# Performance work log

Hardware: AMD Instinct MI355X
Metric: run time of the kernel (lower is better)

Reference implementation:

```python
import jax, jax.numpy as jnp
import numpy as np
from jax import lax

B, S, V, D, L = 16, 512, 32000, 512, 64


def setup_inputs() -> dict:
    key = jax.random.key(0)
    ks = jax.random.split(key, 6)
    return {
        "token_ids": jax.random.randint(ks[0], (B, S), 0, V),
        "vocab_emb": jax.random.normal(ks[1], (V, D), jnp.float32) * 0.02,
        "pos_W": jax.random.normal(ks[2], (D, L), jnp.float32) * (1.0 / np.sqrt(D)),
        "pos_b": jnp.zeros((L,), jnp.float32),
        "W1": jax.random.normal(ks[3], (2 * D, D), jnp.float32) * (1.0 / np.sqrt(2 * D)),
        "b1": jnp.zeros((D,), jnp.float32),
        "w2": jax.random.normal(ks[4], (D,), jnp.float32) * (1.0 / np.sqrt(D)),
        "b2": jnp.zeros((), jnp.float32),
    }


def reference(token_ids, vocab_emb, pos_W, pos_b, W1, b1, w2, b2):
    feats = vocab_emb[token_ids]                      # (B, S, D) embedding lookup
    logits = feats @ pos_W + pos_b                    # (B, S, L) POS-tag logits
    cls = jnp.argmax(logits, axis=-1)                 # (B, S)

    # same_cls_as_neighbor: sequence-chain neighbors OR same predicted class, no self loops
    idx = jnp.arange(S)
    chain = jnp.abs(idx[:, None] - idx[None, :]) == 1
    not_self = idx[:, None] != idx[None, :]
    same = cls[:, :, None] == cls[:, None, :]
    adj = (chain[None] | same) & not_self[None]       # (B, S, S) bool

    # rnn_linear (2D->D) followed directly by rnn_linear2 (D->1) with no nonlinearity:
    # score(i,j) = w2.(W1a f_i + W1b f_j + b1) + b2 = f_i.u + f_j.v + c  (exact rewrite)
    W1a, W1b = W1[:D], W1[D:]
    u = W1a @ w2
    v = W1b @ w2
    c = b1 @ w2 + b2

    def parse_one(f, a):
        # greedy easy-first merge loop: S-1 merges until one node remains
        def step(carry, _):
            f, a, tot = carry
            si = f @ u                                 # (S,)
            sj = f @ v                                 # (S,)
            sc = jnp.where(a, si[:, None] + sj[None, :] + c, -jnp.inf)  # (S, S)
            k = jnp.argmax(sc)                         # flat argmax over neighbor pairs
            i, j = k // S, k % S
            best = sc.reshape(-1)[k]
            parent = f[i] @ W1a + f[j] @ W1b + b1      # parent feature of merged pair
            f = f.at[i].set(parent)                    # slot i <- parent
            row = a[i] | a[j]                          # parent inherits both neighborhoods
            a = a.at[i, :].set(row).at[:, i].set(row)
            a = a.at[j, :].set(False).at[:, j].set(False)  # slot j removed
            a = a.at[i, i].set(False)
            return (f, a, tot + best), jnp.stack([i, j])

        (_, _, tot), tree = lax.scan(step, (f, a, jnp.float32(0.0)), None, length=S - 1)
        return tot, tree

    total_score, parse_tree = jax.vmap(parse_one)(feats, adj)
    return total_score, parse_tree                    # (B,), (B, S-1, 2)
```

## Files before the change

### kernel.cpp

```cpp
#include <hip/hip_runtime.h>

#define cB 16
#define cS 512
#define cD 512
#define cL 64
#define cG 8
#define cT 1024

constexpr size_t FCOPY   = (size_t)cB * cS * cD * 4;
constexpr size_t OFF_F0  = 0;
constexpr size_t OFF_F1  = FCOPY;
constexpr size_t OFF_U   = 2 * FCOPY;
constexpr size_t OFF_V   = OFF_U  + 2048;
constexpr size_t OFF_UA  = OFF_V  + 2048;
constexpr size_t OFF_UB  = OFF_UA + 2048;
constexpr size_t OFF_VA  = OFF_UB + 2048;
constexpr size_t OFF_VB  = OFF_VA + 2048;
constexpr size_t OFF_SC  = OFF_VB + 2048;
constexpr size_t OFF_SI  = OFF_SC + 64;
constexpr size_t OFF_SJ  = OFF_SI + (size_t)cB*cS*4;
constexpr size_t OFF_CLS = OFF_SJ + (size_t)cB*cS*4;
constexpr size_t OFF_ADJ = OFF_CLS+ (size_t)cB*cS*4;
constexpr size_t OFF_RM  = OFF_ADJ+ (size_t)cB*cS*64;
constexpr size_t OFF_RA  = OFF_RM + (size_t)cB*cS*4;
constexpr size_t OFF_BAR = ((OFF_RA + (size_t)cB*cS*4 + 127) & ~(size_t)127);

template <int CTRL, int RMASK>
__device__ __forceinline__ void dpp_max_step(float& v, int& k) {
    const float ov = __int_as_float(__builtin_amdgcn_update_dpp(
        (int)0xff800000u, __float_as_int(v), CTRL, RMASK, 0xf, false));
    const int ok = __builtin_amdgcn_update_dpp(
        0x7fffffff, k, CTRL, RMASK, 0xf, false);
    if (ov > v || (ov == v && ok < k)) { v = ov; k = ok; }
}

__device__ __forceinline__ void wave_max64(float& v, int& k) {
    dpp_max_step<0x111, 0xf>(v, k);
    dpp_max_step<0x112, 0xf>(v, k);
    dpp_max_step<0x114, 0xf>(v, k);
    dpp_max_step<0x118, 0xf>(v, k);
    dpp_max_step<0x142, 0xa>(v, k);
    dpp_max_step<0x143, 0xc>(v, k);
}

template <int N>
__device__ __forceinline__ float dpp_shl_add(float x) {
    const float o = __int_as_float(__builtin_amdgcn_update_dpp(
        0, __float_as_int(x), 0x100 + N , 0xf, 0xf, false));
    return x + o;
}

__global__ void k1_uvc(const float* __restrict__ W1, const float* __restrict__ b1,
                       const float* __restrict__ w2, const float* __restrict__ b2,
                       char* __restrict__ ws) {
    const int t = threadIdx.x;
    const int r = blockIdx.x;
    if (r == 1025) {
        unsigned* bar = (unsigned*)(ws + OFF_BAR);
        for (int i = t; i < 4096; i += 256) bar[i] = 0u;
        return;
    }
    __shared__ float rs[256];
    float acc;
    if (r < 1024) {
        const float* row = W1 + (size_t)r * cD;
        acc = row[t] * w2[t] + row[t + 256] * w2[t + 256];
    } else {
        acc = b1[t] * w2[t] + b1[t + 256] * w2[t + 256];
    }
    rs[t] = acc; __syncthreads();
    for (int o = 128; o; o >>= 1) { if (t < o) rs[t] += rs[t + o]; __syncthreads(); }
    if (t == 0) {
        if (r < 512)        ((float*)(ws + OFF_U))[r] = rs[0];
        else if (r < 1024)  ((float*)(ws + OFF_V))[r - 512] = rs[0];
        else                ((float*)(ws + OFF_SC))[0] = rs[0] + b2[0];
    }
}

__global__ void k1b_proj(const float* __restrict__ W1, const float* __restrict__ b1,
                         char* __restrict__ ws) {
    __shared__ float ru[256], rv[256];
    const int t = threadIdx.x;
    const int k = blockIdx.x;
    const float* U = (const float*)(ws + OFF_U);
    const float* V = (const float*)(ws + OFF_V);
    const float* row = (k < 1024) ? (W1 + (size_t)k * cD) : b1;
    ru[t] = row[t] * U[t] + row[t + 256] * U[t + 256];
    rv[t] = row[t] * V[t] + row[t + 256] * V[t + 256];
    __syncthreads();
    for (int o = 128; o; o >>= 1) {
        if (t < o) { ru[t] += ru[t + o]; rv[t] += rv[t + o]; }
        __syncthreads();
    }
    if (t == 0) {
        if (k < 512)       { ((float*)(ws + OFF_UA))[k] = ru[0]; ((float*)(ws + OFF_VA))[k] = rv[0]; }
        else if (k < 1024) { ((float*)(ws + OFF_UB))[k - 512] = ru[0]; ((float*)(ws + OFF_VB))[k - 512] = rv[0]; }
        else               { ((float*)(ws + OFF_SC))[1] = ru[0]; ((float*)(ws + OFF_SC))[2] = rv[0]; }
    }
}

__global__ void k2_feat(const int* __restrict__ tok, const float* __restrict__ emb,
                        char* __restrict__ ws) {
    __shared__ float ru[256], rv[256];
    const int t = threadIdx.x;
    const int bs = blockIdx.x;
    const float* U = (const float*)(ws + OFF_U);
    const float* V = (const float*)(ws + OFF_V);
    float* F = (float*)(ws + OFF_F0);
    const int tk = tok[bs];
    const float* src = emb + (size_t)tk * cD;
    float* dst = F + (size_t)bs * cD;
    const float e0 = src[t], e1 = src[t + 256];
    dst[t] = e0; dst[t + 256] = e1;
    ru[t] = e0 * U[t] + e1 * U[t + 256];
    rv[t] = e0 * V[t] + e1 * V[t + 256];
    __syncthreads();
    for (int o = 128; o; o >>= 1) {
        if (t < o) { ru[t] += ru[t + o]; rv[t] += rv[t + o]; }
        __syncthreads();
    }
    if (t == 0) {
        ((float*)(ws + OFF_SI))[bs] = ru[0];
        ((float*)(ws + OFF_SJ))[bs] = rv[0];
    }
}

__global__ void k3_cls(const float* __restrict__ posW, const float* __restrict__ posb,
                       char* __restrict__ ws) {
    const int t = threadIdx.x;
    const int bs = blockIdx.x;
    const float* frow = (const float*)(ws + OFF_F0) + (size_t)bs * cD;
    float acc = posb[t];
    for (int k = 0; k < cD; k++) acc += frow[k] * posW[(size_t)k * cL + t];
    int idx = t;
    for (int off = 32; off; off >>= 1) {
        float ov = __shfl_down(acc, off, 64);
        int   oi = __shfl_down(idx, off, 64);
        if (ov > acc || (ov == acc && oi < idx)) { acc = ov; idx = oi; }
    }
    if (t == 0) ((int*)(ws + OFF_CLS))[bs] = idx;
}

__global__ void k4_adj(char* __restrict__ ws) {
    __shared__ float rsv[256]; __shared__ int rsk[256];
    const int t = threadIdx.x;
    const int bs = blockIdx.x;
    const int b = bs >> 9, r = bs & 511;
    const int* cls = (const int*)(ws + OFF_CLS) + (size_t)b * cS;
    const float* SJ = (const float*)(ws + OFF_SJ) + (size_t)b * cS;
    const float sir = ((const float*)(ws + OFF_SI))[bs];
    const float c0 = ((const float*)(ws + OFF_SC))[0];
    unsigned long long* adjrow = (unsigned long long*)(ws + OFF_ADJ) + (size_t)bs * 8;
    const int cr = cls[r];
    float bv = -INFINITY; int bc = 0;
    for (int p = 0; p < 2; p++) {
        const int c = p * 256 + t;
        int dd = c - r; if (dd < 0) dd = -dd;
        const bool allowed = (c != r) && (dd == 1 || cls[c] == cr);
        unsigned long long m = __ballot(allowed);
        if ((t & 63) == 0) adjrow[p * 4 + (t >> 6)] = m;
        if (allowed) {
            float val = sir + SJ[c] + c0;
            if (val > bv || (val == bv && c < bc)) { bv = val; bc = c; }
        }
    }
    rsv[t] = bv; rsk[t] = bc; __syncthreads();
    for (int o = 128; o; o >>= 1) {
        if (t < o) {
            float s2 = rsv[t + o]; int k2 = rsk[t + o];
            if (s2 > rsv[t] || (s2 == rsv[t] && k2 < rsk[t])) { rsv[t] = s2; rsk[t] = k2; }
        }
        __syncthreads();
    }
    if (t == 0) { ((float*)(ws + OFF_RM))[bs] = rsv[0]; ((int*)(ws + OFF_RA))[bs] = rsk[0]; }
}

__global__ void __launch_bounds__(cT, 4)
parse_main(const float* __restrict__ W1, const float* __restrict__ b1,
           char* __restrict__ ws, float* __restrict__ out) {
    const int t  = threadIdx.x;
    const int b  = blockIdx.x & 15;
    const int g  = blockIdx.x >> 4;
    const int d0 = g * 64;
    const int wf = t >> 6;
    const int ln = t & 63;
    const int wv = wf >> 1;
    const int h  = wf & 1;

    unsigned long long* F64[2] = {
        (unsigned long long*)(ws + OFF_F0) + (size_t)b * cS * cD / 2,
        (unsigned long long*)(ws + OFF_F1) + (size_t)b * cS * cD / 2 };
    unsigned* prog = (unsigned*)(ws + OFF_BAR) + (size_t)b * 256;
    const float* SCp = (const float*)(ws + OFF_SC);
    const float c0 = SCp[0], cu_c = SCp[1], cv_c = SCp[2];

    __shared__ unsigned long long AdjL[8 * 512];
    __shared__ float SIl[512], SJl[512], rmax[512];
    __shared__ int   rarg[512];
    __shared__ int   tau[512];
    __shared__ unsigned char par[512];
    __shared__ float rsh[1024];
    __shared__ float wsv[8];  __shared__ int wsk[8];
    __shared__ float ws_si[8], ws_sj[8];
    __shared__ int   s_info;
    __shared__ int   rescanList[516]; __shared__ int nresc;

    const int kbase = wv * 128;
    float wreg[64];
#pragma unroll
    for (int m = 0; m < 32; m++) {
        wreg[2 * m]     = W1[(size_t)(kbase + 4 * m + 2 * h)     * cD + d0 + ln];
        wreg[2 * m + 1] = W1[(size_t)(kbase + 4 * m + 2 * h + 1) * cD + d0 + ln];
    }

    const int xk = (wv & 3) * 128 + 2 * ln;
    float cu0 = 0.f, cu1 = 0.f, cv0 = 0.f, cv1 = 0.f;
    if (h == 0) {
        const float* cu_base = (const float*)(ws + ((wv < 4) ? OFF_UA : OFF_UB));
        const float* cvb     = (const float*)(ws + ((wv < 4) ? OFF_VA : OFF_VB));
        cu0 = cu_base[xk]; cu1 = cu_base[xk + 1];
        cv0 = cvb[xk];     cv1 = cvb[xk + 1];
    }

    if (t < cS) {
        SIl[t]  = ((const float*)(ws + OFF_SI))[b * cS + t];
        SJl[t]  = ((const float*)(ws + OFF_SJ))[b * cS + t];
        rmax[t] = ((const float*)(ws + OFF_RM))[b * cS + t];
        rarg[t] = ((const int*)(ws + OFF_RA))[b * cS + t];
        tau[t]  = -1;
        par[t]  = 0;
        const unsigned long long* AG =
            (const unsigned long long*)(ws + OFF_ADJ) + (size_t)b * cS * 8;
#pragma unroll
        for (int wq = 0; wq < 8; wq++) AdjL[wq * 512 + t] = AG[(size_t)t * 8 + wq];
    }
    float b1v = 0.f;
    if (t < 64) b1v = b1[d0 + t];
    bool myAlive = true;
    float tot = 0.f;
    if (t == 0) nresc = 0;

    if (t < cS) {
        float av = rmax[t]; int ak = (t << 9) | (rarg[t] & 511);
        wave_max64(av, ak);
        if (ln == 63) { wsv[wf] = av; wsk[wf] = ak; }
    }
    __syncthreads();

    for (int it = 0; it < cS - 1; ++it) {
        if (wf == 0) {
            float fv = (ln < 8) ? wsv[ln] : -INFINITY;
            int   fk = (ln < 8) ? wsk[ln] : 0x7fffffff;
            dpp_max_step<0x111, 0xf>(fv, fk);
            dpp_max_step<0x112, 0xf>(fv, fk);
            dpp_max_step<0x114, 0xf>(fv, fk);
            const int bk = __builtin_amdgcn_readlane(fk, 7);
            const int pbi = bk >> 9, pbj = bk & 511;
            const int ti = tau[pbi], tj = tau[pbj];
            const int pi = (int)par[pbi], pj = (int)par[pbj];
            const int need = (ti > tj ? ti : tj) + 1;
            if (need > 0) {
                const unsigned un = (unsigned)need;
                for (;;) {
                    unsigned v = 0xffffffffu;
                    if (ln < 8) v = __hip_atomic_load(prog + ln * 32, __ATOMIC_RELAXED,
                                                      __HIP_MEMORY_SCOPE_AGENT);
                    if (__ballot(v >= un) == ~0ull) break;
                    __builtin_amdgcn_s_sleep(1);
                }
            }
            if (ln == 0) {
                s_info = pbi | (pbj << 9) | (pi << 18) | (pj << 19);
                if (g == 0) {
                    const float bfv = __int_as_float(
                        __builtin_amdgcn_readlane(__float_as_int(fv), 7));
                    tot += bfv;
                    out[16 + b * 1022 + it * 2 + 0] = (float)pbi;
                    out[16 + b * 1022 + it * 2 + 1] = (float)pbj;
                }
            }
        }
        __syncthreads();
        const int info = s_info;
        const int bi = info & 511, bj = (info >> 9) & 511;

        const int myrow  = (wv < 4) ? bi : bj;
        const int mypar  = (wv < 4) ? ((info >> 18) & 1) : ((info >> 19) & 1);
        unsigned long long xv = __hip_atomic_load(
            F64[mypar] + (size_t)myrow * 256 + (wv & 3) * 64 + ln,
            __ATOMIC_RELAXED, __HIP_MEMORY_SCOPE_AGENT);
        float2 f2; __builtin_memcpy(&f2, &xv, 8);
        if (h == 0) {
            float csi = f2.x * cu0 + f2.y * cu1;
            float csj = f2.x * cv0 + f2.y * cv1;
            csi += __shfl_down(csi, 32, 64);  csj += __shfl_down(csj, 32, 64);
            csi += __shfl_down(csi, 16, 64);  csj += __shfl_down(csj, 16, 64);
            csi = dpp_shl_add<8>(csi);  csj = dpp_shl_add<8>(csj);
            csi = dpp_shl_add<4>(csi);  csj = dpp_shl_add<4>(csj);
            csi = dpp_shl_add<2>(csi);  csj = dpp_shl_add<2>(csj);
            csi = dpp_shl_add<1>(csi);  csj = dpp_shl_add<1>(csj);
            if (ln == 0) { ws_si[wv] = csi; ws_sj[wv] = csj; }
        }
        {
            const int ix = __float_as_int(f2.x), iy = __float_as_int(f2.y);
            float aP = 0.f, aQ = 0.f;
            if (h == 0) {
#pragma unroll
                for (int m = 0; m < 32; m++) {
                    const float q0 = __int_as_float(__builtin_amdgcn_readlane(ix, 2 * m));
                    const float q1 = __int_as_float(__builtin_amdgcn_readlane(iy, 2 * m));
                    aP += wreg[2 * m] * q0;
                    aQ += wreg[2 * m + 1] * q1;
                }
            } else {
#pragma unroll
                for (int m = 0; m < 32; m++) {
                    const float q0 = __int_as_float(__builtin_amdgcn_readlane(ix, 2 * m + 1));
                    const float q1 = __int_as_float(__builtin_amdgcn_readlane(iy, 2 * m + 1));
                    aP += wreg[2 * m] * q0;
                    aQ += wreg[2 * m + 1] * q1;
                }
            }
            rsh[t] = aP + aQ;
        }
        __syncthreads();

        if (wf == 0) {
            float p = b1v;
#pragma unroll
            for (int q = 0; q < 8; q++)
                p += rsh[(2 * q) * 64 + ln] + rsh[(2 * q + 1) * 64 + ln];
            __hip_atomic_store((float*)F64[mypar ^ 1] + (size_t)bi * 512 + d0 + ln, p,
                               __ATOMIC_RELAXED, __HIP_MEMORY_SCOPE_AGENT);
        }

        float su = (ln < 8) ? ws_si[ln] : 0.f;
        float sv = (ln < 8) ? ws_sj[ln] : 0.f;
        su = dpp_shl_add<4>(su);  sv = dpp_shl_add<4>(sv);
        su = dpp_shl_add<2>(su);  sv = dpp_shl_add<2>(sv);
        su = dpp_shl_add<1>(su);  sv = dpp_shl_add<1>(sv);
        const float sn = __int_as_float(
            __builtin_amdgcn_readfirstlane(__float_as_int(su))) + cu_c;
        const float jn = __int_as_float(
            __builtin_amdgcn_readfirstlane(__float_as_int(sv))) + cv_c;

        if (t < cS) {
            const float sjn_ = jn;
            const int wbi = bi >> 6, wbj = bj >> 6;
            const unsigned long long mbi = 1ull << (bi & 63), mbj = 1ull << (bj & 63);
            const int r = t;
            if (r == bj) {
                if (myAlive) { myAlive = false; rmax[t] = -INFINITY; }
            } else if (r == bi) {
#pragma unroll
                for (int wq = 0; wq < 8; wq++) {
                    unsigned long long nw = AdjL[wq * 512 + bi] | AdjL[wq * 512 + bj];
                    if (wq == wbi) nw &= ~mbi;
                    if (wq == wbj) nw &= ~mbj;
                    AdjL[wq * 512 + bi] = nw;
                }
                int slot = atomicAdd(&nresc, 1); rescanList[slot] = bi;
                SIl[bi] = sn; SJl[bi] = jn; par[bi] ^= 1; tau[bi] = it;
            } else if (myAlive) {
                unsigned long long wi = AdjL[wbi * 512 + r];
                unsigned long long wj = (wbj == wbi) ? wi : AdjL[wbj * 512 + r];
                const bool nb = ((wi & mbi) | (wj & mbj)) != 0ull;
                if (wbi == wbj) {
                    AdjL[wbi * 512 + r] = (wi & ~(mbi | mbj)) | (nb ? mbi : 0ull);
                } else {
                    AdjL[wbi * 512 + r] = (wi & ~mbi) | (nb ? mbi : 0ull);
                    AdjL[wbj * 512 + r] = wj & ~mbj;
                }
                const int ra = rarg[t];
                if (ra == bi || ra == bj) {
                    int slot = atomicAdd(&nresc, 1); rescanList[slot] = r;
                } else if (nb) {
                    const float val = SIl[r] + sjn_ + c0;
                    if (val > rmax[t] || (val == rmax[t] && bi < ra)) { rmax[t] = val; rarg[t] = bi; }
                }
            }
        }
        if (wf == 0) {
            asm volatile("s_waitcnt vmcnt(0)" ::: "memory");
            if (ln == 0)
                __hip_atomic_store(prog + g * 32, (unsigned)(it + 1), __ATOMIC_RELAXED,
                                   __HIP_MEMORY_SCOPE_AGENT);
        }
        __syncthreads();

        const int nr = nresc;
        for (int q = wf; q < nr; q += 16) {
            const int r = rescanList[q];
            const float sir = SIl[r];
            float bv2 = -INFINITY; int bc2 = 0x7fffffff;
#pragma unroll
            for (int k = 0; k < 8; k++) {
                const unsigned long long word = AdjL[k * 512 + r];
                if ((word >> ln) & 1ull) {
                    const int c = k * 64 + ln;
                    const float val = sir + SJl[c] + c0;
                    if (val > bv2 || (val == bv2 && c < bc2)) { bv2 = val; bc2 = c; }
                }
            }
            wave_max64(bv2, bc2);
            if (ln == 63) { rmax[r] = bv2; rarg[r] = bc2; }
        }
        __syncthreads();

        if (t < cS) {
            float av = rmax[t]; int ak = (t << 9) | (rarg[t] & 511);
            wave_max64(av, ak);
            if (ln == 63) { wsv[wf] = av; wsk[wf] = ak; }
        }
        if (t == 0) nresc = 0;
        __syncthreads();
    }
    if (g == 0 && t == 0) out[b] = tot;
}

extern "C" void kernel_launch(void* const* d_in, const int* in_sizes, int n_in,
                              void* d_out, int out_size, void* d_ws, size_t ws_size,
                              hipStream_t stream) {
    const int*   token_ids = (const int*)d_in[0];
    const float* vocab_emb = (const float*)d_in[1];
    const float* pos_W     = (const float*)d_in[2];
    const float* pos_b     = (const float*)d_in[3];
    const float* W1        = (const float*)d_in[4];
    const float* b1        = (const float*)d_in[5];
    const float* w2        = (const float*)d_in[6];
    const float* b2        = (const float*)d_in[7];
    float* out = (float*)d_out;
    char*  ws  = (char*)d_ws;

    k1_uvc<<<1026, 256, 0, stream>>>(W1, b1, w2, b2, ws);
    k1b_proj<<<1025, 256, 0, stream>>>(W1, b1, ws);
    k2_feat<<<cB * cS, 256, 0, stream>>>(token_ids, vocab_emb, ws);
    k3_cls<<<cB * cS, 64, 0, stream>>>(pos_W, pos_b, ws);
    k4_adj<<<cB * cS, 256, 0, stream>>>(ws);

    void* args[] = { (void*)&W1, (void*)&b1, (void*)&ws, (void*)&out };
    hipLaunchCooperativeKernel((void*)parse_main, dim3(cB * cG), dim3(cT),
                               args, 0, stream);
}
```

Before: 3.035 ms.

## Restructure merge loop to cut a barrier and move parent reduction to idle wave

Removes the per-iteration stage where every wave reduces its row maxima into shared partials. Wave 0 now scans all 512 row maxima itself at the start of the next iteration, which eliminates one __syncthreads per merge step. The parent-feature reduction, global store and progress flag move to wave 15, which does no adjacency update, so that work runs alongside the adjacency update instead of before it. It also caches the last observed progress level to skip redundant spin polls, drops the s_sleep in the spin loop, and uses explicit fmaf with paired weights. The trade-off is a serial 8-element scan per lane on wave 0 and more aggressive polling traffic on the progress counters.

```diff
diff --git a/kernel.cpp b/kernel.cpp
--- a/kernel.cpp
+++ b/kernel.cpp
@@ -200,17 +200,16 @@
     __shared__ int   tau[512];
     __shared__ unsigned char par[512];
     __shared__ float rsh[1024];
-    __shared__ float wsv[8];  __shared__ int wsk[8];
     __shared__ float ws_si[8], ws_sj[8];
     __shared__ int   s_info;
     __shared__ int   rescanList[516]; __shared__ int nresc;
 
     const int kbase = wv * 128;
-    float wreg[64];
+    float2 wreg2[32];
 #pragma unroll
     for (int m = 0; m < 32; m++) {
-        wreg[2 * m]     = W1[(size_t)(kbase + 4 * m + 2 * h)     * cD + d0 + ln];
-        wreg[2 * m + 1] = W1[(size_t)(kbase + 4 * m + 2 * h + 1) * cD + d0 + ln];
+        wreg2[m].x = W1[(size_t)(kbase + 4 * m + 2 * h)     * cD + d0 + ln];
+        wreg2[m].y = W1[(size_t)(kbase + 4 * m + 2 * h + 1) * cD + d0 + ln];
     }
 
     const int xk = (wv & 3) * 128 + 2 * ln;
@@ -235,45 +234,45 @@
         for (int wq = 0; wq < 8; wq++) AdjL[wq * 512 + t] = AG[(size_t)t * 8 + wq];
     }
     float b1v = 0.f;
-    if (t < 64) b1v = b1[d0 + t];
+    if (wf == 15) b1v = b1[d0 + ln];
     bool myAlive = true;
     float tot = 0.f;
+    int minp = 0;
     if (t == 0) nresc = 0;
-
-    if (t < cS) {
-        float av = rmax[t]; int ak = (t << 9) | (rarg[t] & 511);
-        wave_max64(av, ak);
-        if (ln == 63) { wsv[wf] = av; wsk[wf] = ak; }
-    }
     __syncthreads();
 
     for (int it = 0; it < cS - 1; ++it) {
         if (wf == 0) {
-            float fv = (ln < 8) ? wsv[ln] : -INFINITY;
-            int   fk = (ln < 8) ? wsk[ln] : 0x7fffffff;
-            dpp_max_step<0x111, 0xf>(fv, fk);
-            dpp_max_step<0x112, 0xf>(fv, fk);
-            dpp_max_step<0x114, 0xf>(fv, fk);
-            const int bk = __builtin_amdgcn_readlane(fk, 7);
-            const int pbi = bk >> 9, pbj = bk & 511;
+            float bv = -INFINITY; int bk = 0x7fffffff;
+#pragma unroll
+            for (int k = 0; k < 8; k++) {
+                const int r = k * 64 + ln;
+                const float v = rmax[r];
+                const int key = (r << 9) | (rarg[r] & 511);
+                if (v > bv || (v == bv && key < bk)) { bv = v; bk = key; }
+            }
+            wave_max64(bv, bk);
+            const int bk63 = __builtin_amdgcn_readlane(bk, 63);
+            const int pbi = bk63 >> 9, pbj = bk63 & 511;
             const int ti = tau[pbi], tj = tau[pbj];
             const int pi = (int)par[pbi], pj = (int)par[pbj];
             const int need = (ti > tj ? ti : tj) + 1;
-            if (need > 0) {
+            if (need > minp) {
                 const unsigned un = (unsigned)need;
                 for (;;) {
                     unsigned v = 0xffffffffu;
                     if (ln < 8) v = __hip_atomic_load(prog + ln * 32, __ATOMIC_RELAXED,
                                                       __HIP_MEMORY_SCOPE_AGENT);
                     if (__ballot(v >= un) == ~0ull) break;
-                    __builtin_amdgcn_s_sleep(1);
-                }
+                }
+                minp = need;
             }
             if (ln == 0) {
                 s_info = pbi | (pbj << 9) | (pi << 18) | (pj << 19);
+                nresc = 0;
                 if (g == 0) {
                     const float bfv = __int_as_float(
-                        __builtin_amdgcn_readlane(__float_as_int(fv), 7));
+                        __builtin_amdgcn_readlane(__float_as_int(bv), 63));
                     tot += bfv;
                     out[16 + b * 1022 + it * 2 + 0] = (float)pbi;
                     out[16 + b * 1022 + it * 2 + 1] = (float)pbj;
@@ -304,47 +303,41 @@
         {
             const int ix = __float_as_int(f2.x), iy = __float_as_int(f2.y);
             float aP = 0.f, aQ = 0.f;
-            if (h == 0) {
-#pragma unroll
-                for (int m = 0; m < 32; m++) {
-                    const float q0 = __int_as_float(__builtin_amdgcn_readlane(ix, 2 * m));
-                    const float q1 = __int_as_float(__builtin_amdgcn_readlane(iy, 2 * m));
-                    aP += wreg[2 * m] * q0;
-                    aQ += wreg[2 * m + 1] * q1;
-                }
-            } else {
-#pragma unroll
-                for (int m = 0; m < 32; m++) {
-                    const float q0 = __int_as_float(__builtin_amdgcn_readlane(ix, 2 * m + 1));
-                    const float q1 = __int_as_float(__builtin_amdgcn_readlane(iy, 2 * m + 1));
-                    aP += wreg[2 * m] * q0;
-                    aQ += wreg[2 * m + 1] * q1;
-                }
+#pragma unroll
+            for (int m = 0; m < 32; m++) {
+                const int lsrc = 2 * m + h;
+                const float q0 = __int_as_float(__builtin_amdgcn_readlane(ix, lsrc));
+                const float q1 = __int_as_float(__builtin_amdgcn_readlane(iy, lsrc));
+                aP = fmaf(wreg2[m].x, q0, aP);
+                aQ = fmaf(wreg2[m].y, q1, aQ);
             }
             rsh[t] = aP + aQ;
         }
         __syncthreads();
 
-        if (wf == 0) {
+        if (wf == 15) {
+            const int pari = (info >> 18) & 1;
             float p = b1v;
 #pragma unroll
             for (int q = 0; q < 8; q++)
                 p += rsh[(2 * q) * 64 + ln] + rsh[(2 * q + 1) * 64 + ln];
-            __hip_atomic_store((float*)F64[mypar ^ 1] + (size_t)bi * 512 + d0 + ln, p,
+            __hip_atomic_store((float*)F64[pari ^ 1] + (size_t)bi * 512 + d0 + ln, p,
                                __ATOMIC_RELAXED, __HIP_MEMORY_SCOPE_AGENT);
-        }
-
-        float su = (ln < 8) ? ws_si[ln] : 0.f;
-        float sv = (ln < 8) ? ws_sj[ln] : 0.f;
-        su = dpp_shl_add<4>(su);  sv = dpp_shl_add<4>(sv);
-        su = dpp_shl_add<2>(su);  sv = dpp_shl_add<2>(sv);
-        su = dpp_shl_add<1>(su);  sv = dpp_shl_add<1>(sv);
-        const float sn = __int_as_float(
-            __builtin_amdgcn_readfirstlane(__float_as_int(su))) + cu_c;
-        const float jn = __int_as_float(
-            __builtin_amdgcn_readfirstlane(__float_as_int(sv))) + cv_c;
-
-        if (t < cS) {
+            asm volatile("s_waitcnt vmcnt(0)" ::: "memory");
+            if (ln == 0)
+                __hip_atomic_store(prog + g * 32, (unsigned)(it + 1), __ATOMIC_RELAXED,
+                                   __HIP_MEMORY_SCOPE_AGENT);
+        } else if (t < cS) {
+            float su = (ln < 8) ? ws_si[ln] : 0.f;
+            float sv = (ln < 8) ? ws_sj[ln] : 0.f;
+            su = dpp_shl_add<4>(su);  sv = dpp_shl_add<4>(sv);
+            su = dpp_shl_add<2>(su);  sv = dpp_shl_add<2>(sv);
+            su = dpp_shl_add<1>(su);  sv = dpp_shl_add<1>(sv);
+            const float sn = __int_as_float(
+                __builtin_amdgcn_readfirstlane(__float_as_int(su))) + cu_c;
+            const float jn = __int_as_float(
+                __builtin_amdgcn_readfirstlane(__float_as_int(sv))) + cv_c;
+
             const float sjn_ = jn;
             const int wbi = bi >> 6, wbj = bj >> 6;
             const unsigned long long mbi = 1ull << (bi & 63), mbj = 1ull << (bj & 63);
@@ -380,12 +373,6 @@
                 }
             }
         }
-        if (wf == 0) {
-            asm volatile("s_waitcnt vmcnt(0)" ::: "memory");
-            if (ln == 0)
-                __hip_atomic_store(prog + g * 32, (unsigned)(it + 1), __ATOMIC_RELAXED,
-                                   __HIP_MEMORY_SCOPE_AGENT);
-        }
         __syncthreads();
 
         const int nr = nresc;
@@ -405,14 +392,6 @@
             wave_max64(bv2, bc2);
             if (ln == 63) { rmax[r] = bv2; rarg[r] = bc2; }
         }
-        __syncthreads();
-
-        if (t < cS) {
-            float av = rmax[t]; int ak = (t << 9) | (rarg[t] & 511);
-            wave_max64(av, ak);
-            if (ln == 63) { wsv[wf] = av; wsk[wf] = ak; }
-        }
-        if (t == 0) nresc = 0;
         __syncthreads();
     }
     if (g == 0 && t == 0) out[b] = tot;
```

New measurement: 3.491 ms. +15.0%, slower.
